# Performance work log

Hardware: AMD Instinct MI355X
Metric: run time of the kernel (lower is better)

The kernel has to match this reference:

```python
import math
import jax, jax.numpy as jnp
import numpy as np

# irreps_in == irreps_out == 256x0e + 256x1o + 128x2e
# (start, end, mul, ir_dim) for each irrep block in the flat feature vector
SEGS = [(0, 256, 256, 1), (256, 1024, 256, 3), (1024, 1664, 128, 5)]
DIM = 1664
BATCH = 32768
NW = sum(m * m for _, _, m, _ in SEGS)  # 147456
NB = 256  # bias only on scalar (0e) output


def setup_inputs() -> dict:
    key = jax.random.key(0)
    k1, k2, k3 = jax.random.split(key, 3)
    ws = jax.random.normal(k1, (NW,), dtype=jnp.float32)
    bs = jax.random.normal(k2, (NB,), dtype=jnp.float32)
    x = jax.random.normal(k3, (BATCH, DIM), dtype=jnp.float32)
    return {"ws": ws, "bs": bs, "x": x}


def reference(ws, bs, x):
    # Block-diagonal equivariant linear. Each instruction:
    #   out[i_out] += einsum('uw,ui->wi', w, x_block) / sqrt(mul_in * fan_in)
    # Here in/out irreps match 1:1, so fan_in = 1 for every output.
    w_off = 0
    outs = []
    for (s, e, mul, d) in SEGS:
        w = ws[w_off:w_off + mul * mul].reshape(mul, mul)
        w_off += mul * mul
        xb = x[:, s:e].reshape(-1, mul, d)  # [B, u, i]
        o = jnp.einsum('uw,bui->bwi', w, xb) * (1.0 / math.sqrt(mul))
        outs.append(o.reshape(-1, mul * d))
    # bias on the scalar (0e) output block only
    outs[0] = outs[0] + bs
    return jnp.concatenate(outs, axis=-1)  # [B, 1664]
```

## Files before the change

### kernel.cpp

```cpp
#include <hip/hip_runtime.h>


typedef short short8 __attribute__((ext_vector_type(8)));
typedef short short4v __attribute__((ext_vector_type(4)));
typedef float f32x4 __attribute__((ext_vector_type(4)));

#define DIMF 1664

__device__ __forceinline__ unsigned short f2bf(float f) {
  unsigned int u = __float_as_uint(f);
  u += 0x7fffu + ((u >> 16) & 1u);
  return (unsigned short)(u >> 16);
}

__global__ __launch_bounds__(256) void prep_w(const float* __restrict__ ws,
                                              unsigned short* __restrict__ wf) {
  int t = blockIdx.x * blockDim.x + threadIdx.x;
  int MUL, woff, goff;
  float scale;
  if (t < 8192) {
    MUL = 256; woff = 0; goff = 0; scale = 0.0625f;
  } else if (t < 16384) {
    MUL = 256; woff = 65536; goff = 8192; scale = 0.0625f;
  } else if (t < 18432) {
    MUL = 128; woff = 131072; goff = 16384; scale = 0.088388347648318447f;
  } else {
    return;
  }
  int g = t - goff;
  int l = g & 63;
  int nks = MUL >> 5;
  int ks = (g >> 6) % nks;
  int nt = g / (64 * nks);
  int n = nt * 16 + (l & 15);
  int kb = ks * 32 + (l >> 4) * 8;
  short8 v;
#pragma unroll
  for (int j = 0; j < 8; ++j)
    v[j] = (short)f2bf(ws[woff + (size_t)(kb + j) * MUL + n] * scale);
  *reinterpret_cast<short8*>(wf + (size_t)t * 8) = v;
}

template <int MUL, int D, int BMB, bool BIAS>
__device__ __forceinline__ void gemm_seg(const float* __restrict__ x,
                                         const unsigned short* __restrict__ wf,
                                         const float* __restrict__ bs,
                                         float* __restrict__ out, int blk, int s,
                                         unsigned short* A_lds) {
  constexpr int LDA = MUL + 8;
  constexpr int MT = BMB * D;
  constexpr int NMT = MT / 16;
  constexpr int NTW = MUL / 64;
  constexpr int NKS = MUL / 32;
  constexpr int QPR = MUL / 4;
  constexpr int NQ = BMB * QPR / 256;

  const int tid = threadIdx.x;
  const int lane = tid & 63;
  const int wave = tid >> 6;
  const int l15 = lane & 15;
  const int lhi = lane >> 4;
  const int b0 = blk * BMB;

  {
    int g = tid;
#pragma unroll
    for (int it = 0; it < NQ; ++it, g += 256) {
      int r = g / QPR;
      int q = g - r * QPR;
      const float* src = x + (size_t)(b0 + r) * DIMF + s + q * 4 * D;
      f32x4 v[D];
#pragma unroll
      for (int jd = 0; jd < D; ++jd)
        v[jd] = reinterpret_cast<const f32x4*>(src)[jd];
#pragma unroll
      for (int i = 0; i < D; ++i) {
        short4v p;
#pragma unroll
        for (int up = 0; up < 4; ++up) {
          int j = up * D + i;
          p[up] = (short)f2bf(v[j >> 2][j & 3]);
        }
        *reinterpret_cast<short4v*>(&A_lds[(r * D + i) * LDA + q * 4]) = p;
      }
    }
  }
  __syncthreads();

  f32x4 acc[NMT][NTW];
#pragma unroll
  for (int a = 0; a < NMT; ++a)
#pragma unroll
    for (int b = 0; b < NTW; ++b) acc[a][b] = (f32x4){0.f, 0.f, 0.f, 0.f};

  for (int ks = 0; ks < NKS; ++ks) {
    short8 af[NMT];
#pragma unroll
    for (int mt = 0; mt < NMT; ++mt)
      af[mt] = *reinterpret_cast<const short8*>(
          &A_lds[(mt * 16 + l15) * LDA + ks * 32 + lhi * 8]);
#pragma unroll
    for (int nt = 0; nt < NTW; ++nt) {
      int ntg = wave * NTW + nt;
      short8 bfr = *reinterpret_cast<const short8*>(
          wf + ((size_t)(ntg * NKS + ks) * 64 + lane) * 8);
#pragma unroll
      for (int mt = 0; mt < NMT; ++mt)
        acc[mt][nt] =
            __builtin_amdgcn_mfma_f32_16x16x32_bf16(af[mt], bfr, acc[mt][nt], 0, 0, 0);
    }
  }

#pragma unroll
  for (int nt = 0; nt < NTW; ++nt) {
    int n = wave * (MUL / 4) + nt * 16 + l15;
    float bias = 0.f;
    if (BIAS) bias = bs[n];
#pragma unroll
    for (int mt = 0; mt < NMT; ++mt) {
#pragma unroll
      for (int q = 0; q < 4; ++q) {
        int m = mt * 16 + lhi * 4 + q;
        int b = m / D;
        int i = m - b * D;
        out[(size_t)(b0 + b) * DIMF + s + n * D + i] = acc[mt][nt][q] + bias;
      }
    }
  }
}

__global__ __launch_bounds__(256) void linear_main(const float* __restrict__ x,
                                                   const unsigned short* __restrict__ wf,
                                                   const float* __restrict__ bs,
                                                   float* __restrict__ out) {
  __shared__ unsigned short A_lds[48 * 264];
  int blk = blockIdx.x;
  if (blk < 1024) {
    gemm_seg<256, 1, 32, true>(x, wf, bs, out, blk, 0, A_lds);
  } else if (blk < 3072) {
    gemm_seg<256, 3, 16, false>(x, wf + 65536, bs, out, blk - 1024, 256, A_lds);
  } else {
    gemm_seg<128, 5, 16, false>(x, wf + 131072, bs, out, blk - 3072, 1024, A_lds);
  }
}

extern "C" void kernel_launch(void* const* d_in, const int* in_sizes, int n_in,
                              void* d_out, int out_size, void* d_ws, size_t ws_size,
                              hipStream_t stream) {
  const float* ws = (const float*)d_in[0];
  const float* bs = (const float*)d_in[1];
  const float* x = (const float*)d_in[2];
  float* out = (float*)d_out;
  unsigned short* wf = (unsigned short*)d_ws;

  hipLaunchKernelGGL(prep_w, dim3(72), dim3(256), 0, stream, ws, wf);
  hipLaunchKernelGGL(linear_main, dim3(1024 + 2048 + 2048), dim3(256), 0, stream, x,
                     wf, bs, out);
}
```

Before: 120.5 us.

## Make GEMM persistent with register-resident weights and LDS-staged coalesced epilogue

The kernel becomes persistent: 512 blocks of 512 threads, each looping over batch tiles of its irrep segment. Each wave loads its slice of the packed bf16 weights into registers once and reuses it for every tile. Input loads become fully coalesced float4 reads, with the u/i transpose done through scattered LDS writes. For the vector and tensor segments, outputs are staged through an LDS buffer so global stores are contiguous float4 writes rather than strided scalars. The cost is higher register and LDS use, plus a fixed block split across segments that may leave load imbalance.

Measured after the change: 223.7 us. +85.7%, slower.

```diff
diff --git a/kernel.cpp b/kernel.cpp
--- a/kernel.cpp
+++ b/kernel.cpp
@@ -42,105 +42,141 @@
 }
 
 template <int MUL, int D, int BMB, bool BIAS>
-__device__ __forceinline__ void gemm_seg(const float* __restrict__ x,
-                                         const unsigned short* __restrict__ wf,
-                                         const float* __restrict__ bs,
-                                         float* __restrict__ out, int blk, int s,
-                                         unsigned short* A_lds) {
+__device__ __forceinline__ void seg_run(const float* __restrict__ x,
+                                        const unsigned short* __restrict__ wf,
+                                        const float* __restrict__ bs,
+                                        float* __restrict__ out, int t0, int NT,
+                                        int nblk, int s, char* lds) {
   constexpr int LDA = MUL + 8;
+  constexpr int LDN = MUL + 2;
   constexpr int MT = BMB * D;
   constexpr int NMT = MT / 16;
-  constexpr int NTW = MUL / 64;
+  constexpr int NTW = MUL / 128;
   constexpr int NKS = MUL / 32;
-  constexpr int QPR = MUL / 4;
-  constexpr int NQ = BMB * QPR / 256;
+  constexpr int NFR = NTW * NKS;
+  constexpr int CPR = MUL * D / 4;
+  constexpr int NG = BMB * CPR / 512;
+
+  unsigned short* A = (unsigned short*)lds;
+  float* E = (float*)(lds + MT * LDA * 2);
 
   const int tid = threadIdx.x;
   const int lane = tid & 63;
   const int wave = tid >> 6;
   const int l15 = lane & 15;
   const int lhi = lane >> 4;
-  const int b0 = blk * BMB;
 
-  {
-    int g = tid;
+  short8 wfr[NFR];
 #pragma unroll
-    for (int it = 0; it < NQ; ++it, g += 256) {
-      int r = g / QPR;
-      int q = g - r * QPR;
-      const float* src = x + (size_t)(b0 + r) * DIMF + s + q * 4 * D;
-      f32x4 v[D];
+  for (int nt = 0; nt < NTW; ++nt)
 #pragma unroll
-      for (int jd = 0; jd < D; ++jd)
-        v[jd] = reinterpret_cast<const f32x4*>(src)[jd];
+    for (int ks = 0; ks < NKS; ++ks) {
+      int ntg = wave * NTW + nt;
+      wfr[nt * NKS + ks] = *reinterpret_cast<const short8*>(
+          wf + ((size_t)(ntg * NKS + ks) * 64 + lane) * 8);
+    }
+
+  for (int t = t0; t < NT; t += nblk) {
+    const int b0 = t * BMB;
 #pragma unroll
-      for (int i = 0; i < D; ++i) {
+    for (int it = 0; it < NG; ++it) {
+      int g = tid + it * 512;
+      int r = g / CPR;
+      int c4 = g - r * CPR;
+      f32x4 v = *reinterpret_cast<const f32x4*>(x + (size_t)(b0 + r) * DIMF + s + c4 * 4);
+      if (D == 1) {
         short4v p;
 #pragma unroll
-        for (int up = 0; up < 4; ++up) {
-          int j = up * D + i;
-          p[up] = (short)f2bf(v[j >> 2][j & 3]);
+        for (int j = 0; j < 4; ++j) p[j] = (short)f2bf(v[j]);
+        *reinterpret_cast<short4v*>(&A[r * LDA + c4 * 4]) = p;
+      } else {
+#pragma unroll
+        for (int j = 0; j < 4; ++j) {
+          int col = c4 * 4 + j;
+          int u = col / D;
+          int i = col - u * D;
+          A[(r * D + i) * LDA + u] = f2bf(v[j]);
         }
-        *reinterpret_cast<short4v*>(&A_lds[(r * D + i) * LDA + q * 4]) = p;
       }
     }
-  }
-  __syncthreads();
+    __syncthreads();
 
-  f32x4 acc[NMT][NTW];
+    f32x4 acc[NMT][NTW];
 #pragma unroll
-  for (int a = 0; a < NMT; ++a)
+    for (int a = 0; a < NMT; ++a)
 #pragma unroll
-    for (int b = 0; b < NTW; ++b) acc[a][b] = (f32x4){0.f, 0.f, 0.f, 0.f};
-
-  for (int ks = 0; ks < NKS; ++ks) {
-    short8 af[NMT];
+      for (int b = 0; b < NTW; ++b) acc[a][b] = (f32x4){0.f, 0.f, 0.f, 0.f};
 #pragma unroll
-    for (int mt = 0; mt < NMT; ++mt)
-      af[mt] = *reinterpret_cast<const short8*>(
-          &A_lds[(mt * 16 + l15) * LDA + ks * 32 + lhi * 8]);
-#pragma unroll
-    for (int nt = 0; nt < NTW; ++nt) {
-      int ntg = wave * NTW + nt;
-      short8 bfr = *reinterpret_cast<const short8*>(
-          wf + ((size_t)(ntg * NKS + ks) * 64 + lane) * 8);
+    for (int ks = 0; ks < NKS; ++ks) {
+      short8 af[NMT];
 #pragma unroll
       for (int mt = 0; mt < NMT; ++mt)
-        acc[mt][nt] =
-            __builtin_amdgcn_mfma_f32_16x16x32_bf16(af[mt], bfr, acc[mt][nt], 0, 0, 0);
+        af[mt] = *reinterpret_cast<const short8*>(
+            &A[(mt * 16 + l15) * LDA + ks * 32 + lhi * 8]);
+#pragma unroll
+      for (int nt = 0; nt < NTW; ++nt)
+#pragma unroll
+        for (int mt = 0; mt < NMT; ++mt)
+          acc[mt][nt] = __builtin_amdgcn_mfma_f32_16x16x32_bf16(af[mt], wfr[nt * NKS + ks],
+                                                                acc[mt][nt], 0, 0, 0);
     }
-  }
 
+    if (BIAS) {
 #pragma unroll
-  for (int nt = 0; nt < NTW; ++nt) {
-    int n = wave * (MUL / 4) + nt * 16 + l15;
-    float bias = 0.f;
-    if (BIAS) bias = bs[n];
+      for (int nt = 0; nt < NTW; ++nt) {
+        int n = (wave * NTW + nt) * 16 + l15;
+        float bias = bs[n];
 #pragma unroll
-    for (int mt = 0; mt < NMT; ++mt) {
+        for (int mt = 0; mt < NMT; ++mt)
 #pragma unroll
-      for (int q = 0; q < 4; ++q) {
-        int m = mt * 16 + lhi * 4 + q;
-        int b = m / D;
-        int i = m - b * D;
-        out[(size_t)(b0 + b) * DIMF + s + n * D + i] = acc[mt][nt][q] + bias;
+          for (int q = 0; q < 4; ++q) {
+            int m = mt * 16 + lhi * 4 + q;
+            out[(size_t)(b0 + m) * DIMF + s + n] = acc[mt][nt][q] + bias;
+          }
+      }
+      __syncthreads();
+    } else {
+#pragma unroll
+      for (int nt = 0; nt < NTW; ++nt) {
+        int n = (wave * NTW + nt) * 16 + l15;
+#pragma unroll
+        for (int mt = 0; mt < NMT; ++mt)
+#pragma unroll
+          for (int q = 0; q < 4; ++q)
+            E[(mt * 16 + lhi * 4 + q) * LDN + n] = acc[mt][nt][q];
+      }
+      __syncthreads();
+#pragma unroll
+      for (int it = 0; it < NG; ++it) {
+        int g = tid + it * 512;
+        int r = g / CPR;
+        int c4 = g - r * CPR;
+        f32x4 o;
+#pragma unroll
+        for (int j = 0; j < 4; ++j) {
+          int c = c4 * 4 + j;
+          int w = c / D;
+          int i = c - w * D;
+          o[j] = E[(r * D + i) * LDN + w];
+        }
+        *reinterpret_cast<f32x4*>(out + (size_t)(b0 + r) * DIMF + s + c4 * 4) = o;
       }
     }
   }
 }
 
-__global__ __launch_bounds__(256) void linear_main(const float* __restrict__ x,
-                                                   const unsigned short* __restrict__ wf,
-                                                   const float* __restrict__ bs,
-                                                   float* __restrict__ out) {
-  __shared__ unsigned short A_lds[48 * 264];
+__global__ __launch_bounds__(512, 4) void linear_main(const float* __restrict__ x,
+                                                      const unsigned short* __restrict__ wf,
+                                                      const float* __restrict__ bs,
+                                                      float* __restrict__ out) {
+  __shared__ __align__(16) char lds[25344 + 49536];
   int blk = blockIdx.x;
-  if (blk < 1024) {
-    gemm_seg<256, 1, 32, true>(x, wf, bs, out, blk, 0, A_lds);
-  } else if (blk < 3072) {
-    gemm_seg<256, 3, 16, false>(x, wf + 65536, bs, out, blk - 1024, 256, A_lds);
+  if (blk < 80) {
+    seg_run<256, 1, 32, true>(x, wf, bs, out, blk, 1024, 80, 0, lds);
+  } else if (blk < 316) {
+    seg_run<256, 3, 16, false>(x, wf + 65536, bs, out, blk - 80, 2048, 236, 256, lds);
   } else {
-    gemm_seg<128, 5, 16, false>(x, wf + 131072, bs, out, blk - 3072, 1024, A_lds);
+    seg_run<128, 5, 16, false>(x, wf + 131072, bs, out, blk - 316, 2048, 196, 1024, lds);
   }
 }
 
@@ -154,6 +190,5 @@
   unsigned short* wf = (unsigned short*)d_ws;
 
   hipLaunchKernelGGL(prep_w, dim3(72), dim3(256), 0, stream, ws, wf);
-  hipLaunchKernelGGL(linear_main, dim3(1024 + 2048 + 2048), dim3(256), 0, stream, x,
-                     wf, bs, out);
+  hipLaunchKernelGGL(linear_main, dim3(512), dim3(512), 0, stream, x, wf, bs, out);
 }
```

## Load x tiles directly into LDS as fp32 and convert to bf16 at fragment read

Applied to the files above, without the earlier changes.

Replaces the register-staged load-convert-store of the x tile with global_load_lds direct-to-LDS copies of raw fp32 rows, padded per group to avoid bank conflicts. The bf16 conversion and the u/i deinterleave move into the MFMA fragment loads, which now read strided fp32 from LDS, and the k-loop is fully unrolled. The goal is to cut VGPR pressure and issue overhead in the load phase. In exchange the LDS footprint doubles, which may reduce occupancy, and each k-step repeats the conversion with strided scalar LDS reads for D>1.

After: 127.8 us. 1.06x slower.

```diff
diff --git a/kernel.cpp b/kernel.cpp
--- a/kernel.cpp
+++ b/kernel.cpp
@@ -2,7 +2,6 @@
 
 
 typedef short short8 __attribute__((ext_vector_type(8)));
-typedef short short4v __attribute__((ext_vector_type(4)));
 typedef float f32x4 __attribute__((ext_vector_type(4)));
 
 #define DIMF 1664
@@ -11,6 +10,12 @@
   unsigned int u = __float_as_uint(f);
   u += 0x7fffu + ((u >> 16) & 1u);
   return (unsigned short)(u >> 16);
+}
+
+__device__ __forceinline__ void gload16(const float* g, float* l) {
+  __builtin_amdgcn_global_load_lds(
+      (const __attribute__((address_space(1))) void*)g,
+      (__attribute__((address_space(3))) void*)l, 16, 0, 0);
 }
 
 __global__ __launch_bounds__(256) void prep_w(const float* __restrict__ ws,
@@ -41,19 +46,20 @@
   *reinterpret_cast<short8*>(wf + (size_t)t * 8) = v;
 }
 
-template <int MUL, int D, int BMB, bool BIAS>
-__device__ __forceinline__ void gemm_seg(const float* __restrict__ x,
-                                         const unsigned short* __restrict__ wf,
-                                         const float* __restrict__ bs,
-                                         float* __restrict__ out, int blk, int s,
-                                         unsigned short* A_lds) {
-  constexpr int LDA = MUL + 8;
+template <int MUL, int D, int BMB, int GR, int GSF, bool BIAS>
+__device__ __forceinline__ void seg_run(const float* __restrict__ x,
+                                        const unsigned short* __restrict__ wf,
+                                        const float* __restrict__ bs,
+                                        float* __restrict__ out, int blk, int s,
+                                        float* A32) {
+  constexpr int SEGW = MUL * D;
+  constexpr int ISS = GR * SEGW / 256;
+  constexpr int NGRP = BMB / GR;
+  constexpr int NISS = NGRP * ISS;
   constexpr int MT = BMB * D;
   constexpr int NMT = MT / 16;
   constexpr int NTW = MUL / 64;
   constexpr int NKS = MUL / 32;
-  constexpr int QPR = MUL / 4;
-  constexpr int NQ = BMB * QPR / 256;
 
   const int tid = threadIdx.x;
   const int lane = tid & 63;
@@ -62,30 +68,25 @@
   const int lhi = lane >> 4;
   const int b0 = blk * BMB;
 
-  {
-    int g = tid;
+  for (int m = wave; m < NISS; m += 4) {
+    int g = m / ISS;
+    int j = m - g * ISS;
+    int q = j * 256 + lane * 4;
+    int r = g * GR + q / SEGW;
+    int c = q % SEGW;
+    gload16(x + (size_t)(b0 + r) * DIMF + s + c, A32 + g * GSF + j * 256);
+  }
+  asm volatile("s_waitcnt vmcnt(0)" ::: "memory");
+  __syncthreads();
+
+  int rowoff[NMT];
 #pragma unroll
-    for (int it = 0; it < NQ; ++it, g += 256) {
-      int r = g / QPR;
-      int q = g - r * QPR;
-      const float* src = x + (size_t)(b0 + r) * DIMF + s + q * 4 * D;
-      f32x4 v[D];
-#pragma unroll
-      for (int jd = 0; jd < D; ++jd)
-        v[jd] = reinterpret_cast<const f32x4*>(src)[jd];
-#pragma unroll
-      for (int i = 0; i < D; ++i) {
-        short4v p;
-#pragma unroll
-        for (int up = 0; up < 4; ++up) {
-          int j = up * D + i;
-          p[up] = (short)f2bf(v[j >> 2][j & 3]);
-        }
-        *reinterpret_cast<short4v*>(&A_lds[(r * D + i) * LDA + q * 4]) = p;
-      }
-    }
+  for (int mt = 0; mt < NMT; ++mt) {
+    int ar = mt * 16 + l15;
+    int b = ar / D;
+    int i = ar - b * D;
+    rowoff[mt] = (b / GR) * GSF + (b % GR) * SEGW + i;
   }
-  __syncthreads();
 
   f32x4 acc[NMT][NTW];
 #pragma unroll
@@ -93,12 +94,26 @@
 #pragma unroll
     for (int b = 0; b < NTW; ++b) acc[a][b] = (f32x4){0.f, 0.f, 0.f, 0.f};
 
+#pragma unroll
   for (int ks = 0; ks < NKS; ++ks) {
     short8 af[NMT];
 #pragma unroll
-    for (int mt = 0; mt < NMT; ++mt)
-      af[mt] = *reinterpret_cast<const short8*>(
-          &A_lds[(mt * 16 + l15) * LDA + ks * 32 + lhi * 8]);
+    for (int mt = 0; mt < NMT; ++mt) {
+      if (D == 1) {
+        f32x4 lo = *reinterpret_cast<const f32x4*>(&A32[rowoff[mt] + ks * 32 + lhi * 8]);
+        f32x4 hi =
+            *reinterpret_cast<const f32x4*>(&A32[rowoff[mt] + ks * 32 + lhi * 8 + 4]);
+#pragma unroll
+        for (int j = 0; j < 4; ++j) {
+          af[mt][j] = (short)f2bf(lo[j]);
+          af[mt][j + 4] = (short)f2bf(hi[j]);
+        }
+      } else {
+#pragma unroll
+        for (int j = 0; j < 8; ++j)
+          af[mt][j] = (short)f2bf(A32[rowoff[mt] + (ks * 32 + lhi * 8 + j) * D]);
+      }
+    }
 #pragma unroll
     for (int nt = 0; nt < NTW; ++nt) {
       int ntg = wave * NTW + nt;
@@ -133,14 +148,14 @@
                                                    const unsigned short* __restrict__ wf,
                                                    const float* __restrict__ bs,
                                                    float* __restrict__ out) {
-  __shared__ unsigned short A_lds[48 * 264];
+  __shared__ __align__(16) float A32[12352];
   int blk = blockIdx.x;
   if (blk < 1024) {
-    gemm_seg<256, 1, 32, true>(x, wf, bs, out, blk, 0, A_lds);
+    seg_run<256, 1, 32, 1, 260, true>(x, wf, bs, out, blk, 0, A32);
   } else if (blk < 3072) {
-    gemm_seg<256, 3, 16, false>(x, wf + 65536, bs, out, blk - 1024, 256, A_lds);
+    seg_run<256, 3, 16, 1, 772, false>(x, wf + 65536, bs, out, blk - 1024, 256, A32);
   } else {
-    gemm_seg<128, 5, 16, false>(x, wf + 131072, bs, out, blk - 3072, 1024, A_lds);
+    seg_run<128, 5, 16, 2, 1288, false>(x, wf + 131072, bs, out, blk - 3072, 1024, A32);
   }
 }
 
```

## Make blocks persistent over four tiles with double-buffered LDS prefetch

Applied to the files above, without the earlier changes.

Each block now handles four consecutive row tiles instead of one. The LDS A buffer is double-buffered so the global loads for the next tile are issued before the MFMA compute of the current one, overlapping memory latency with compute. The global load was also changed to fully contiguous float4 reads, with a scalar scatter/transpose into LDS for D>1 segments, and the grid shrinks to 1280 blocks with launch_bounds occupancy hint 3. Costs include more registers for prefetched tiles and twice the LDS per block. The scalar LDS writes may also cause bank conflicts.

Result: slower. 222.5 us (+84.7%).

```diff
diff --git a/kernel.cpp b/kernel.cpp
--- a/kernel.cpp
+++ b/kernel.cpp
@@ -41,106 +41,139 @@
   *reinterpret_cast<short8*>(wf + (size_t)t * 8) = v;
 }
 
-template <int MUL, int D, int BMB, bool BIAS>
-__device__ __forceinline__ void gemm_seg(const float* __restrict__ x,
-                                         const unsigned short* __restrict__ wf,
-                                         const float* __restrict__ bs,
-                                         float* __restrict__ out, int blk, int s,
-                                         unsigned short* A_lds) {
+template <int MUL, int D, int BMB, int TPB, bool BIAS>
+__device__ __forceinline__ void seg_run(const float* __restrict__ x,
+                                        const unsigned short* __restrict__ wf,
+                                        const float* __restrict__ bs,
+                                        float* __restrict__ out, int blk, int s,
+                                        unsigned short* Ab) {
   constexpr int LDA = MUL + 8;
   constexpr int MT = BMB * D;
   constexpr int NMT = MT / 16;
   constexpr int NTW = MUL / 64;
   constexpr int NKS = MUL / 32;
-  constexpr int QPR = MUL / 4;
-  constexpr int NQ = BMB * QPR / 256;
+  constexpr int CPR = MUL * D / 4;
+  constexpr int NG = BMB * CPR / 256;
+  constexpr int BUF = MT * LDA;
 
   const int tid = threadIdx.x;
   const int lane = tid & 63;
   const int wave = tid >> 6;
   const int l15 = lane & 15;
   const int lhi = lane >> 4;
-  const int b0 = blk * BMB;
+  const int t0 = blk * TPB;
+
+  float bias[NTW];
+  if (BIAS) {
+#pragma unroll
+    for (int nt = 0; nt < NTW; ++nt) bias[nt] = bs[(wave * NTW + nt) * 16 + l15];
+  }
+
+  auto load_tile = [&](int b0, f32x4* v) {
+#pragma unroll
+    for (int it = 0; it < NG; ++it) {
+      int g = tid + it * 256;
+      int r = g / CPR;
+      int c = (g - r * CPR) * 4;
+      v[it] = *reinterpret_cast<const f32x4*>(x + (size_t)(b0 + r) * DIMF + s + c);
+    }
+  };
+
+  auto write_tile = [&](const f32x4* v, unsigned short* A) {
+#pragma unroll
+    for (int it = 0; it < NG; ++it) {
+      int g = tid + it * 256;
+      int r = g / CPR;
+      int c = (g - r * CPR) * 4;
+      if (D == 1) {
+        short4v p;
+#pragma unroll
+        for (int j = 0; j < 4; ++j) p[j] = (short)f2bf(v[it][j]);
+        *reinterpret_cast<short4v*>(&A[r * LDA + c]) = p;
+      } else {
+        int u0 = c / D;
+        int i0 = c - u0 * D;
+#pragma unroll
+        for (int j = 0; j < 4; ++j) {
+          int ii = i0 + j;
+          int u = u0;
+          if (ii >= D) { ii -= D; ++u; }
+          A[(r * D + ii) * LDA + u] = f2bf(v[it][j]);
+        }
+      }
+    }
+  };
+
+  auto compute_store = [&](int b0, const unsigned short* A) {
+    f32x4 acc[NMT][NTW];
+#pragma unroll
+    for (int a = 0; a < NMT; ++a)
+#pragma unroll
+      for (int b = 0; b < NTW; ++b) acc[a][b] = (f32x4){0.f, 0.f, 0.f, 0.f};
+#pragma unroll
+    for (int ks = 0; ks < NKS; ++ks) {
+      short8 af[NMT];
+#pragma unroll
+      for (int mt = 0; mt < NMT; ++mt)
+        af[mt] = *reinterpret_cast<const short8*>(
+            &A[(mt * 16 + l15) * LDA + ks * 32 + lhi * 8]);
+#pragma unroll
+      for (int nt = 0; nt < NTW; ++nt) {
+        int ntg = wave * NTW + nt;
+        short8 bfr = *reinterpret_cast<const short8*>(
+            wf + ((size_t)(ntg * NKS + ks) * 64 + lane) * 8);
+#pragma unroll
+        for (int mt = 0; mt < NMT; ++mt)
+          acc[mt][nt] = __builtin_amdgcn_mfma_f32_16x16x32_bf16(af[mt], bfr,
+                                                                acc[mt][nt], 0, 0, 0);
+      }
+    }
+#pragma unroll
+    for (int nt = 0; nt < NTW; ++nt) {
+      int n = wave * (MUL / 4) + nt * 16 + l15;
+      float bi = BIAS ? bias[nt] : 0.f;
+#pragma unroll
+      for (int mt = 0; mt < NMT; ++mt)
+#pragma unroll
+        for (int q = 0; q < 4; ++q) {
+          int m = mt * 16 + lhi * 4 + q;
+          int b = m / D;
+          int i = m - b * D;
+          out[(size_t)(b0 + b) * DIMF + s + n * D + i] = acc[mt][nt][q] + bi;
+        }
+    }
+  };
 
   {
-    int g = tid;
-#pragma unroll
-    for (int it = 0; it < NQ; ++it, g += 256) {
-      int r = g / QPR;
-      int q = g - r * QPR;
-      const float* src = x + (size_t)(b0 + r) * DIMF + s + q * 4 * D;
-      f32x4 v[D];
-#pragma unroll
-      for (int jd = 0; jd < D; ++jd)
-        v[jd] = reinterpret_cast<const f32x4*>(src)[jd];
-#pragma unroll
-      for (int i = 0; i < D; ++i) {
-        short4v p;
-#pragma unroll
-        for (int up = 0; up < 4; ++up) {
-          int j = up * D + i;
-          p[up] = (short)f2bf(v[j >> 2][j & 3]);
-        }
-        *reinterpret_cast<short4v*>(&A_lds[(r * D + i) * LDA + q * 4]) = p;
-      }
-    }
+    f32x4 v[NG];
+    load_tile(t0 * BMB, v);
+    write_tile(v, Ab);
   }
   __syncthreads();
 
-  f32x4 acc[NMT][NTW];
 #pragma unroll
-  for (int a = 0; a < NMT; ++a)
-#pragma unroll
-    for (int b = 0; b < NTW; ++b) acc[a][b] = (f32x4){0.f, 0.f, 0.f, 0.f};
-
-  for (int ks = 0; ks < NKS; ++ks) {
-    short8 af[NMT];
-#pragma unroll
-    for (int mt = 0; mt < NMT; ++mt)
-      af[mt] = *reinterpret_cast<const short8*>(
-          &A_lds[(mt * 16 + l15) * LDA + ks * 32 + lhi * 8]);
-#pragma unroll
-    for (int nt = 0; nt < NTW; ++nt) {
-      int ntg = wave * NTW + nt;
-      short8 bfr = *reinterpret_cast<const short8*>(
-          wf + ((size_t)(ntg * NKS + ks) * 64 + lane) * 8);
-#pragma unroll
-      for (int mt = 0; mt < NMT; ++mt)
-        acc[mt][nt] =
-            __builtin_amdgcn_mfma_f32_16x16x32_bf16(af[mt], bfr, acc[mt][nt], 0, 0, 0);
-    }
-  }
-
-#pragma unroll
-  for (int nt = 0; nt < NTW; ++nt) {
-    int n = wave * (MUL / 4) + nt * 16 + l15;
-    float bias = 0.f;
-    if (BIAS) bias = bs[n];
-#pragma unroll
-    for (int mt = 0; mt < NMT; ++mt) {
-#pragma unroll
-      for (int q = 0; q < 4; ++q) {
-        int m = mt * 16 + lhi * 4 + q;
-        int b = m / D;
-        int i = m - b * D;
-        out[(size_t)(b0 + b) * DIMF + s + n * D + i] = acc[mt][nt][q] + bias;
-      }
-    }
+  for (int tt = 0; tt < TPB; ++tt) {
+    unsigned short* Acur = Ab + (tt & 1) * BUF;
+    f32x4 v[NG];
+    if (tt + 1 < TPB) load_tile((t0 + tt + 1) * BMB, v);
+    compute_store((t0 + tt) * BMB, Acur);
+    if (tt + 1 < TPB) write_tile(v, Ab + ((tt + 1) & 1) * BUF);
+    __syncthreads();
   }
 }
 
-__global__ __launch_bounds__(256) void linear_main(const float* __restrict__ x,
-                                                   const unsigned short* __restrict__ wf,
-                                                   const float* __restrict__ bs,
-                                                   float* __restrict__ out) {
-  __shared__ unsigned short A_lds[48 * 264];
+__global__ __launch_bounds__(256, 3) void linear_main(const float* __restrict__ x,
+                                                      const unsigned short* __restrict__ wf,
+                                                      const float* __restrict__ bs,
+                                                      float* __restrict__ out) {
+  __shared__ __align__(16) unsigned short A[2 * 12672];
   int blk = blockIdx.x;
-  if (blk < 1024) {
-    gemm_seg<256, 1, 32, true>(x, wf, bs, out, blk, 0, A_lds);
-  } else if (blk < 3072) {
-    gemm_seg<256, 3, 16, false>(x, wf + 65536, bs, out, blk - 1024, 256, A_lds);
+  if (blk < 256) {
+    seg_run<256, 1, 32, 4, true>(x, wf, bs, out, blk, 0, A);
+  } else if (blk < 768) {
+    seg_run<256, 3, 16, 4, false>(x, wf + 65536, bs, out, blk - 256, 256, A);
   } else {
-    gemm_seg<128, 5, 16, false>(x, wf + 131072, bs, out, blk - 3072, 1024, A_lds);
+    seg_run<128, 5, 16, 4, false>(x, wf + 131072, bs, out, blk - 768, 1024, A);
   }
 }
 
@@ -154,6 +187,5 @@
   unsigned short* wf = (unsigned short*)d_ws;
 
   hipLaunchKernelGGL(prep_w, dim3(72), dim3(256), 0, stream, ws, wf);
-  hipLaunchKernelGGL(linear_main, dim3(1024 + 2048 + 2048), dim3(256), 0, stream, x,
-                     wf, bs, out);
+  hipLaunchKernelGGL(linear_main, dim3(1280), dim3(256), 0, stream, x, wf, bs, out);
 }
```
